# Kernel tuning notes

Hardware: AMD Instinct MI355X
Metric: run time of the kernel (lower is better)

The kernel has to match this reference:

```python
import jax, jax.numpy as jnp
import numpy as np
import itertools as it
from math import factorial

DIM, N = 3, 30
K = 2 * DIM * N + 1          # 181
P = factorial(N) // factorial(N - DIM)  # 24360
DEMB = DIM * DIM + K         # 190

# permutation index tables (trace-time constants)
_combs = np.array(list(it.permutations(range(N), DIM)), dtype=np.int32)          # (P, DIM)
_rest = np.array([sorted(set(range(N)) - set(map(int, c))) for c in _combs],
                 dtype=np.int32)                                                  # (P, N-DIM)


def setup_inputs() -> dict:
    key = jax.random.key(0)
    k0, k1, k2, k3, k4 = jax.random.split(key, 5)
    return {
        "matrix": jax.random.normal(k0, (DIM, N), dtype=jnp.float32),
        "Ws_in": jax.random.normal(k1, (K, DIM), dtype=jnp.float32),        # inner weights_sort
        "Wd_in": jax.random.normal(k2, (K, N - DIM), dtype=jnp.float32),    # inner weights_dot
        "Ws_out": jax.random.normal(k3, (K, DEMB), dtype=jnp.float32),      # outer weights_sort
        "Wd_out": jax.random.normal(k4, (K, P), dtype=jnp.float32),         # outer weights_dot
    }


def reference(matrix, Ws_in, Wd_in, Ws_out, Wd_out):
    combs = jnp.asarray(_combs)   # (P, DIM)
    rest = jnp.asarray(_rest)     # (P, N-DIM)
    cols = matrix.T               # (N, DIM) -- columns of the cloud as rows

    # UpperGram, batched over all P permutations
    Xd = cols[combs].transpose(0, 2, 1)   # (P, DIM, DIM) selected columns
    Xr = cols[rest].transpose(0, 2, 1)    # (P, DIM, N-DIM) remaining columns (sorted)
    gram = jnp.einsum('pdi,pdj->pij', Xd, Xd)          # Xd^T Xd, (P, DIM, DIM)
    # torch flattens gram.transpose(1,0); gram is exactly symmetric so this equals row-major
    gram_flat = gram.transpose(0, 2, 1).reshape(P, DIM * DIM)
    proj = jnp.einsum('pdi,pdm->pim', Xd, Xr)          # Xd^T Xrest, (P, DIM, N-DIM)

    # inner Embed (non-original branch), batched over P
    sm = jnp.einsum('pim,ki->pmk', proj, Ws_in)        # (P, N-DIM, K)
    sm_sorted = jnp.sort(sm, axis=1)                   # column-wise sort (dim=0 in torch)
    emb = jnp.einsum('km,pmk->pk', Wd_in, sm_sorted)   # diag(Wd @ sorted), (P, K)

    vec = jnp.concatenate([gram_flat, emb], axis=1)    # (P, DEMB); torch's vec before .t()

    # outer Embed (original branch) on mat = vec.T (DEMB, P)
    sm2 = vec @ Ws_out.T                               # mat^T @ Ws^T, (P, K)
    sm2_sorted = jnp.sort(sm2, axis=0)                 # sort over permutation axis
    out = jnp.einsum('kp,pk->k', Wd_out, sm2_sorted)   # diag(Wd @ sorted), (K,)
    return out
```

## Files before the change

### kernel.cpp

```cpp
#include <hip/hip_runtime.h>
#include <hip/hip_bf16.h>

#define DIMK 3
#define NPTS 30
#define KK   181
#define PP   24360
#define DEMB 190
#define VLD  192
#define SNP  24576
#define SNPS 24608

typedef __attribute__((ext_vector_type(8))) short bf16x8;
typedef __attribute__((ext_vector_type(4))) float f32x4;
typedef __attribute__((ext_vector_type(2))) __fp16 h2;
typedef __attribute__((ext_vector_type(4))) ushort u16x4;
typedef __attribute__((ext_vector_type(4))) unsigned u32x4;

__device__ __forceinline__ ushort f2bf(float f) {
    unsigned u = __float_as_uint(f);
    u += 0x7FFFu + ((u >> 16) & 1u);
    return (ushort)(u >> 16);
}

__global__ __launch_bounds__(1024, 2) void k_inner(
    const float* __restrict__ M,
    const float* __restrict__ Ws_in,
    const float* __restrict__ Wd_in,
    const float* __restrict__ Wout,
    ushort* __restrict__ Abf,
    ushort* __restrict__ vec)
{
    __shared__ float Gs[NPTS * 32];
    __shared__ float WsS[192 * 3];
    __shared__ float WdS[192 * 28];

    const int tid = threadIdx.x;

    {
        int gid = blockIdx.x * 1024 + tid;
        if (gid < 192 * 192) {
            int k = gid / 192, d = gid - k * 192;
            Abf[gid] = (k < KK && d < DEMB) ? f2bf(Wout[k * DEMB + d]) : (ushort)0;
        }
    }

    for (int i = tid; i < 192 * 3; i += 1024) WsS[i] = (i < KK * 3) ? Ws_in[i] : 0.f;
    for (int i = tid; i < 192 * 28; i += 1024) {
        int k = i / 28, m = i - k * 28;
        WdS[i] = (k < KK && m < 27) ? Wd_in[k * 27 + m] : 0.f;
    }
    for (int e = tid; e < NPTS * 32; e += 1024) {
        int a = e >> 5, b = e & 31;
        Gs[e] = (b < NPTS)
            ? (M[a] * M[b] + M[NPTS + a] * M[NPTS + b] + M[2 * NPTS + a] * M[2 * NPTS + b])
            : 0.f;
    }
    __syncthreads();

    const int wave = __builtin_amdgcn_readfirstlane(tid >> 6);
    const int lane = tid & 63;
    const int wid = blockIdx.x * 16 + wave;
    const int chunk = wid % 3;
    const int pstream = wid / 3;
    const int nstream = (chunk == 2) ? 2730 : 2731;
    const int k = chunk * 64 + lane;

    const float INF = __builtin_inff();
    const bool kvalid = (k < KK);
    const float w0 = WsS[k * 3 + 0];
    const float w1 = WsS[k * 3 + 1];
    const float w2 = WsS[k * 3 + 2];
    const float* wd = WdS + k * 28;

    const int NPAIR = PP / 2;

    for (int t = pstream; t < NPAIR; t += nstream) {
        const int p0 = 2 * t;
        int i0 = p0 / 812;
        int r  = p0 - i0 * 812;
        int i1 = r / 28;
        int i2 = r - i1 * 28;
        int c0 = i0;
        int c1 = i1 + (i1 >= c0 ? 1 : 0);
        int lo = min(c0, c1), hi = max(c0, c1);
        int c2a = i2;
        if (c2a >= lo) c2a++;
        if (c2a >= hi) c2a++;
        int c2b = i2 + 1;
        if (c2b >= lo) c2b++;
        if (c2b >= hi) c2b++;

        ushort* vrow0 = vec + (long)p0 * VLD;
        ushort* vrow1 = vrow0 + VLD;

        if (chunk == 0 && lane < 9) {
            int i = lane / 3, j = lane % 3;
            int cia = (i == 0) ? c0 : ((i == 1) ? c1 : c2a);
            int cja = (j == 0) ? c0 : ((j == 1) ? c1 : c2a);
            vrow0[lane] = f2bf(Gs[(cia << 5) + cja]);
            int cib = (i == 0) ? c0 : ((i == 1) ? c1 : c2b);
            int cjb = (j == 0) ? c0 : ((j == 1) ? c1 : c2b);
            vrow1[lane] = f2bf(Gs[(cib << 5) + cjb]);
        }

        const float* g0 = Gs + (c0 << 5);
        const float* g1 = Gs + (c1 << 5);
        const float* ga = Gs + (c2a << 5);
        const float* gb = Gs + (c2b << 5);
        const unsigned basem = (1u << c0) | (1u << c1);
        const unsigned maska = basem | (1u << c2a);
        const unsigned maskb = basem | (1u << c2b);

        h2 s[30];
#pragma unroll
        for (int q = 0; q < 8; ++q) {
            float4 x0 = *(const float4*)&g0[q * 4];
            float4 x1 = *(const float4*)&g1[q * 4];
            float4 xa = *(const float4*)&ga[q * 4];
            float4 xb = *(const float4*)&gb[q * 4];
            int j0 = q * 4;
            if (j0 + 0 < NPTS) {
                float c = w0 * x0.x + w1 * x1.x;
                float va = w2 * xa.x + c;
                float vb = w2 * xb.x + c;
                va = ((maska >> (j0 + 0)) & 1u) ? INF : va;
                vb = ((maskb >> (j0 + 0)) & 1u) ? INF : vb;
                s[j0 + 0] = __builtin_amdgcn_cvt_pkrtz(va, vb);
            }
            if (j0 + 1 < NPTS) {
                float c = w0 * x0.y + w1 * x1.y;
                float va = w2 * xa.y + c;
                float vb = w2 * xb.y + c;
                va = ((maska >> (j0 + 1)) & 1u) ? INF : va;
                vb = ((maskb >> (j0 + 1)) & 1u) ? INF : vb;
                s[j0 + 1] = __builtin_amdgcn_cvt_pkrtz(va, vb);
            }
            if (j0 + 2 < NPTS) {
                float c = w0 * x0.z + w1 * x1.z;
                float va = w2 * xa.z + c;
                float vb = w2 * xb.z + c;
                va = ((maska >> (j0 + 2)) & 1u) ? INF : va;
                vb = ((maskb >> (j0 + 2)) & 1u) ? INF : vb;
                s[j0 + 2] = __builtin_amdgcn_cvt_pkrtz(va, vb);
            }
            if (j0 + 3 < NPTS) {
                float c = w0 * x0.w + w1 * x1.w;
                float va = w2 * xa.w + c;
                float vb = w2 * xb.w + c;
                va = ((maska >> (j0 + 3)) & 1u) ? INF : va;
                vb = ((maskb >> (j0 + 3)) & 1u) ? INF : vb;
                s[j0 + 3] = __builtin_amdgcn_cvt_pkrtz(va, vb);
            }
        }

#pragma unroll
        for (int pw = 1; pw < 32; pw <<= 1) {
#pragma unroll
            for (int kk = pw; kk >= 1; kk >>= 1) {
#pragma unroll
                for (int j = kk % pw; j + kk < 32; j += 2 * kk) {
#pragma unroll
                    for (int i = 0; i < kk; ++i) {
                        int a = i + j, b = i + j + kk;
                        if (a / (pw * 2) == b / (pw * 2) && b < 30
                            && !(pw == 16 && a == 27)) {
                            h2 x = s[a], y = s[b];
                            s[a] = __builtin_elementwise_min(x, y);
                            s[b] = __builtin_elementwise_max(x, y);
                        }
                    }
                }
            }
        }

        if (kvalid) {
            float emb0 = 0.f, emb1 = 0.f;
#pragma unroll
            for (int j = 0; j < 24; j += 4) {
                float4 w4 = *(const float4*)&wd[j];
                emb0 += w4.x * (float)s[j + 0].x + w4.y * (float)s[j + 1].x
                      + w4.z * (float)s[j + 2].x + w4.w * (float)s[j + 3].x;
                emb1 += w4.x * (float)s[j + 0].y + w4.y * (float)s[j + 1].y
                      + w4.z * (float)s[j + 2].y + w4.w * (float)s[j + 3].y;
            }
            {
                float4 w4 = *(const float4*)&wd[24];
                emb0 += w4.x * (float)s[24].x + w4.y * (float)s[25].x
                      + w4.z * (float)s[26].x;
                emb1 += w4.x * (float)s[24].y + w4.y * (float)s[25].y
                      + w4.z * (float)s[26].y;
            }
            vrow0[9 + k] = f2bf(emb0);
            vrow1[9 + k] = f2bf(emb1);
        } else if (k < 183) {
            vrow0[9 + k] = 0;
            vrow1[9 + k] = 0;
        }
    }
}

__global__ __launch_bounds__(256) void k_gemm(
    const ushort* __restrict__ vecB,
    const ushort* __restrict__ Abf,
    ushort* __restrict__ sm2TP)
{
    const int tid  = threadIdx.x;
    const int bid  = blockIdx.x;
    const int tile = bid >> 2;
    const int qtr  = bid & 3;
    const int wave = tid >> 6;
    const int lane = tid & 63;
    const int n = lane & 15;
    const int quad = lane >> 4;

    const int prow = tile * 64 + wave * 16 + n;
    bf16x8 afrag[6];
    {
        const ushort* row = vecB + (size_t)prow * VLD;
#pragma unroll
        for (int kc = 0; kc < 6; ++kc)
            afrag[kc] = *(const bf16x8*)&row[kc * 32 + quad * 8];
    }

    const int pb = tile * 64 + wave * 16 + quad * 4;

#pragma unroll
    for (int i = 0; i < 3; ++i) {
        const int kt = qtr * 3 + i;
        const int kg = kt * 16 + n;
        f32x4 acc = {0.f, 0.f, 0.f, 0.f};
        const ushort* arow = Abf + kg * 192;
#pragma unroll
        for (int kc = 0; kc < 6; ++kc) {
            bf16x8 bfrag = *(const bf16x8*)&arow[kc * 32 + quad * 8];
            acc = __builtin_amdgcn_mfma_f32_16x16x32_bf16(afrag[kc], bfrag, acc, 0, 0, 0);
        }
        if (kg < KK) {
            u16x4 st;
#pragma unroll
            for (int r = 0; r < 4; ++r) {
                int p = pb + r;
                unsigned e;
                if (p < PP) {
                    unsigned u = __float_as_uint(acc[r]);
                    u = (u & 0x80000000u) ? ~u : (u | 0x80000000u);
                    e = (u + 0x8000u) >> 16;
                } else {
                    e = 0xFFFFu;
                }
                st[r] = (ushort)e;
            }
            *(u16x4*)&sm2TP[(size_t)kg * SNPS + pb] = st;
        }
    }
}

__global__ __launch_bounds__(1024, 1) void k_hist(
    const ushort* __restrict__ sm2TP,
    const float* __restrict__ WdOut,
    float* __restrict__ out)
{
    __shared__ unsigned hist[16384];
    __shared__ ushort sv[SNP];
    __shared__ unsigned wred[16];
    __shared__ float fred[16];

    const int tid  = threadIdx.x;
    const int wave = tid >> 6;
    const int lane = tid & 63;
    const int k    = blockIdx.x;

    const ushort* rowU = sm2TP + (size_t)k * SNPS;
    const float* wrow  = WdOut + (size_t)k * PP;

    u16x4 kv[6];
#pragma unroll
    for (int j = 0; j < 6; ++j)
        kv[j] = *(const u16x4*)&rowU[tid * 4 + j * 4096];

    unsigned below = 0;
    for (int p2 = 0; p2 < 2; ++p2) {
        const unsigned kbase = (unsigned)p2 << 15;

        for (int i = tid; i < 4096; i += 1024)
            ((u32x4*)hist)[i] = (u32x4){0u, 0u, 0u, 0u};
        __syncthreads();

#pragma unroll
        for (int j = 0; j < 6; ++j) {
#pragma unroll
            for (int e = 0; e < 4; ++e) {
                unsigned u = kv[j][e];
                unsigned rel = u - kbase;
                if (rel < 32768u) {
                    unsigned wd = rel >> 1;
                    atomicAdd(&hist[((wd & 15u) << 10) + (wd >> 4)],
                              1u << ((rel & 1u) << 4));
                }
            }
        }
        __syncthreads();

        unsigned w[16];
        unsigned tsum = 0;
#pragma unroll
        for (int i = 0; i < 16; ++i) {
            w[i] = hist[(i << 10) + tid];
            tsum += (w[i] & 0xFFFFu) + (w[i] >> 16);
        }
        unsigned inc = tsum;
#pragma unroll
        for (int off = 1; off < 64; off <<= 1) {
            unsigned o = (unsigned)__shfl_up((int)inc, off, 64);
            if (lane >= off) inc += o;
        }
        if (lane == 63) wred[wave] = inc;
        __syncthreads();
        unsigned wbase = 0, tot = 0;
#pragma unroll
        for (int ww = 0; ww < 16; ++ww) {
            unsigned t = wred[ww];
            tot += t;
            wbase += (ww < wave) ? t : 0u;
        }

        unsigned running = below + wbase + (inc - tsum);
#pragma unroll
        for (int i = 0; i < 16; ++i) {
            unsigned lob = running;
            running += (w[i] & 0xFFFFu);
            unsigned hib = running;
            running += (w[i] >> 16);
            hist[(i << 10) + tid] = lob | (hib << 16);
        }
        __syncthreads();

#pragma unroll
        for (int j = 0; j < 6; ++j) {
#pragma unroll
            for (int e = 0; e < 4; ++e) {
                unsigned u = kv[j][e];
                unsigned rel = u - kbase;
                if (rel < 32768u) {
                    unsigned wd = rel >> 1;
                    unsigned sh = (rel & 1u) << 4;
                    unsigned old = atomicAdd(&hist[((wd & 15u) << 10) + (wd >> 4)],
                                             1u << sh);
                    unsigned r = (old >> sh) & 0xFFFFu;
                    unsigned raw16 = (u & 0x8000u) ? (u & 0x7FFFu)
                                                   : ((~u) & 0xFFFFu);
                    sv[r] = (ushort)raw16;
                }
            }
        }
        below += tot;
        __syncthreads();
    }

    float acc = 0.f;
#pragma unroll
    for (int j = 0; j < 6; ++j) {
        int i4 = tid * 4 + j * 4096;
        if (i4 < PP) {
            u16x4 s4 = *(const u16x4*)&sv[i4];
            float4 w4 = *(const float4*)&wrow[i4];
            acc += w4.x * __uint_as_float((unsigned)s4[0] << 16)
                 + w4.y * __uint_as_float((unsigned)s4[1] << 16)
                 + w4.z * __uint_as_float((unsigned)s4[2] << 16)
                 + w4.w * __uint_as_float((unsigned)s4[3] << 16);
        }
    }

#pragma unroll
    for (int off = 32; off > 0; off >>= 1)
        acc += __shfl_down(acc, off, 64);
    if (lane == 0) fred[wave] = acc;
    __syncthreads();
    if (tid == 0) {
        float t = 0.f;
#pragma unroll
        for (int ww = 0; ww < 16; ++ww) t += fred[ww];
        out[k] = t;
    }
}

extern "C" void kernel_launch(void* const* d_in, const int* in_sizes, int n_in,
                              void* d_out, int out_size, void* d_ws, size_t ws_size,
                              hipStream_t stream) {
    const float* M      = (const float*)d_in[0];
    const float* Ws_in  = (const float*)d_in[1];
    const float* Wd_in  = (const float*)d_in[2];
    const float* Ws_out = (const float*)d_in[3];
    const float* Wd_out = (const float*)d_in[4];
    float* out = (float*)d_out;

    char* ws = (char*)d_ws;
    ushort* vecB  = (ushort*)ws;
    ushort* Abf   = (ushort*)(ws + (size_t)PP * VLD * 2);
    ushort* sm2TP = (ushort*)(ws + (size_t)PP * VLD * 2 + (size_t)192 * 192 * 2);

    k_inner<<<512, 1024, 0, stream>>>(M, Ws_in, Wd_in, Ws_out, Abf, vecB);

    k_gemm<<<(SNP / 64) * 4, 256, 0, stream>>>(vecB, Abf, sm2TP);

    k_hist<<<KK, 1024, 0, stream>>>(sm2TP, Wd_out, out);
}
```

Measured before the change: 160.4 us.

## Split per-row counting sort across four blocks by key range with atomic output

The histogram/counting-sort kernel now runs four blocks per output row. Each block handles one quarter of the 16-bit key range, so it needs a smaller histogram and a single pass. Each block counts the keys below its range to find its offset, scatters only its own keys, and dots them against the matching slice of Wd_out. Partial results are combined with atomicAdd into an output zeroed by the GEMM kernel. This raises parallelism from 181 blocks to 724 and cuts shared memory per block, at the cost of every block re-reading the full row and a non-deterministic float accumulation order.

```diff
diff --git a/kernel.cpp b/kernel.cpp
--- a/kernel.cpp
+++ b/kernel.cpp
@@ -202,7 +202,8 @@
 __global__ __launch_bounds__(256) void k_gemm(
     const ushort* __restrict__ vecB,
     const ushort* __restrict__ Abf,
-    ushort* __restrict__ sm2TP)
+    ushort* __restrict__ sm2TP,
+    float* __restrict__ out)
 {
     const int tid  = threadIdx.x;
     const int bid  = blockIdx.x;
@@ -212,6 +213,8 @@
     const int lane = tid & 63;
     const int n = lane & 15;
     const int quad = lane >> 4;
+
+    if (bid == 0 && tid < KK) out[tid] = 0.f;
 
     const int prow = tile * 64 + wave * 16 + n;
     bf16x8 afrag[6];
@@ -255,132 +258,128 @@
     }
 }
 
-__global__ __launch_bounds__(1024, 1) void k_hist(
+__global__ __launch_bounds__(1024, 8) void k_hist(
     const ushort* __restrict__ sm2TP,
     const float* __restrict__ WdOut,
     float* __restrict__ out)
 {
-    __shared__ unsigned hist[16384];
+    __shared__ unsigned hist[8192];
     __shared__ ushort sv[SNP];
-    __shared__ unsigned wred[16];
-    __shared__ float fred[16];
+    unsigned* scr = (unsigned*)sv;
 
     const int tid  = threadIdx.x;
     const int wave = tid >> 6;
     const int lane = tid & 63;
-    const int k    = blockIdx.x;
+    const int k = blockIdx.x >> 2;
+    const int q = blockIdx.x & 3;
+    const unsigned qbase = (unsigned)q << 14;
 
     const ushort* rowU = sm2TP + (size_t)k * SNPS;
     const float* wrow  = WdOut + (size_t)k * PP;
 
+    for (int i = tid; i < 2048; i += 1024)
+        ((u32x4*)hist)[i] = (u32x4){0u, 0u, 0u, 0u};
+    __syncthreads();
+
     u16x4 kv[6];
-#pragma unroll
-    for (int j = 0; j < 6; ++j)
+    unsigned below = 0;
+#pragma unroll
+    for (int j = 0; j < 6; ++j) {
         kv[j] = *(const u16x4*)&rowU[tid * 4 + j * 4096];
-
-    unsigned below = 0;
-    for (int p2 = 0; p2 < 2; ++p2) {
-        const unsigned kbase = (unsigned)p2 << 15;
-
-        for (int i = tid; i < 4096; i += 1024)
-            ((u32x4*)hist)[i] = (u32x4){0u, 0u, 0u, 0u};
-        __syncthreads();
-
-#pragma unroll
-        for (int j = 0; j < 6; ++j) {
-#pragma unroll
-            for (int e = 0; e < 4; ++e) {
-                unsigned u = kv[j][e];
-                unsigned rel = u - kbase;
-                if (rel < 32768u) {
-                    unsigned wd = rel >> 1;
-                    atomicAdd(&hist[((wd & 15u) << 10) + (wd >> 4)],
-                              1u << ((rel & 1u) << 4));
-                }
-            }
-        }
-        __syncthreads();
-
-        unsigned w[16];
-        unsigned tsum = 0;
-#pragma unroll
-        for (int i = 0; i < 16; ++i) {
-            w[i] = hist[(i << 10) + tid];
-            tsum += (w[i] & 0xFFFFu) + (w[i] >> 16);
-        }
-        unsigned inc = tsum;
-#pragma unroll
-        for (int off = 1; off < 64; off <<= 1) {
-            unsigned o = (unsigned)__shfl_up((int)inc, off, 64);
-            if (lane >= off) inc += o;
-        }
-        if (lane == 63) wred[wave] = inc;
-        __syncthreads();
-        unsigned wbase = 0, tot = 0;
-#pragma unroll
-        for (int ww = 0; ww < 16; ++ww) {
-            unsigned t = wred[ww];
-            tot += t;
-            wbase += (ww < wave) ? t : 0u;
-        }
-
-        unsigned running = below + wbase + (inc - tsum);
-#pragma unroll
-        for (int i = 0; i < 16; ++i) {
-            unsigned lob = running;
-            running += (w[i] & 0xFFFFu);
-            unsigned hib = running;
-            running += (w[i] >> 16);
-            hist[(i << 10) + tid] = lob | (hib << 16);
-        }
-        __syncthreads();
-
-#pragma unroll
-        for (int j = 0; j < 6; ++j) {
-#pragma unroll
-            for (int e = 0; e < 4; ++e) {
-                unsigned u = kv[j][e];
-                unsigned rel = u - kbase;
-                if (rel < 32768u) {
-                    unsigned wd = rel >> 1;
-                    unsigned sh = (rel & 1u) << 4;
-                    unsigned old = atomicAdd(&hist[((wd & 15u) << 10) + (wd >> 4)],
-                                             1u << sh);
-                    unsigned r = (old >> sh) & 0xFFFFu;
-                    unsigned raw16 = (u & 0x8000u) ? (u & 0x7FFFu)
-                                                   : ((~u) & 0xFFFFu);
-                    sv[r] = (ushort)raw16;
-                }
-            }
-        }
-        below += tot;
-        __syncthreads();
-    }
+#pragma unroll
+        for (int e = 0; e < 4; ++e) {
+            unsigned u = kv[j][e];
+            unsigned rel = u - qbase;
+            if (rel < 16384u) {
+                unsigned wd = rel >> 1;
+                atomicAdd(&hist[((wd & 7u) << 10) + (wd >> 3)],
+                          1u << ((rel & 1u) << 4));
+            } else {
+                below += (u < qbase) ? 1u : 0u;
+            }
+        }
+    }
+#pragma unroll
+    for (int off = 32; off > 0; off >>= 1)
+        below += (unsigned)__shfl_down((int)below, off, 64);
+    if (lane == 0) scr[wave] = below;
+    __syncthreads();
+    unsigned below_tot = 0;
+#pragma unroll
+    for (int ww = 0; ww < 16; ++ww) below_tot += scr[ww];
+    __syncthreads();
+
+    unsigned w[8];
+    unsigned tsum = 0;
+#pragma unroll
+    for (int i = 0; i < 8; ++i) {
+        w[i] = hist[(i << 10) + tid];
+        tsum += (w[i] & 0xFFFFu) + (w[i] >> 16);
+    }
+    unsigned inc = tsum;
+#pragma unroll
+    for (int off = 1; off < 64; off <<= 1) {
+        unsigned o = (unsigned)__shfl_up((int)inc, off, 64);
+        if (lane >= off) inc += o;
+    }
+    if (lane == 63) scr[wave] = inc;
+    __syncthreads();
+    unsigned wbase = 0, tot = 0;
+#pragma unroll
+    for (int ww = 0; ww < 16; ++ww) {
+        unsigned t = scr[ww];
+        tot += t;
+        wbase += (ww < wave) ? t : 0u;
+    }
+    __syncthreads();
+
+    unsigned running = wbase + (inc - tsum);
+#pragma unroll
+    for (int i = 0; i < 8; ++i) {
+        unsigned lob = running;
+        running += (w[i] & 0xFFFFu);
+        unsigned hib = running;
+        running += (w[i] >> 16);
+        hist[(i << 10) + tid] = lob | (hib << 16);
+    }
+    __syncthreads();
+
+#pragma unroll
+    for (int j = 0; j < 6; ++j) {
+#pragma unroll
+        for (int e = 0; e < 4; ++e) {
+            unsigned u = kv[j][e];
+            unsigned rel = u - qbase;
+            if (rel < 16384u) {
+                unsigned wd = rel >> 1;
+                unsigned sh = (rel & 1u) << 4;
+                unsigned old = atomicAdd(&hist[((wd & 7u) << 10) + (wd >> 3)],
+                                         1u << sh);
+                unsigned r = (old >> sh) & 0xFFFFu;
+                unsigned raw16 = (u & 0x8000u) ? (u & 0x7FFFu)
+                                               : ((~u) & 0xFFFFu);
+                sv[r] = (ushort)raw16;
+            }
+        }
+    }
+    __syncthreads();
 
     float acc = 0.f;
-#pragma unroll
-    for (int j = 0; j < 6; ++j) {
-        int i4 = tid * 4 + j * 4096;
-        if (i4 < PP) {
-            u16x4 s4 = *(const u16x4*)&sv[i4];
-            float4 w4 = *(const float4*)&wrow[i4];
-            acc += w4.x * __uint_as_float((unsigned)s4[0] << 16)
-                 + w4.y * __uint_as_float((unsigned)s4[1] << 16)
-                 + w4.z * __uint_as_float((unsigned)s4[2] << 16)
-                 + w4.w * __uint_as_float((unsigned)s4[3] << 16);
-        }
-    }
+    int cap = min((int)tot, PP - (int)below_tot);
+    for (int i = tid; i < cap; i += 1024)
+        acc += wrow[below_tot + i] * __uint_as_float((unsigned)sv[i] << 16);
 
 #pragma unroll
     for (int off = 32; off > 0; off >>= 1)
         acc += __shfl_down(acc, off, 64);
-    if (lane == 0) fred[wave] = acc;
+    __syncthreads();
+    if (lane == 0) ((float*)scr)[wave] = acc;
     __syncthreads();
     if (tid == 0) {
         float t = 0.f;
 #pragma unroll
-        for (int ww = 0; ww < 16; ++ww) t += fred[ww];
-        out[k] = t;
+        for (int ww = 0; ww < 16; ++ww) t += ((float*)scr)[ww];
+        atomicAdd(&out[k], t);
     }
 }
 
@@ -401,7 +400,7 @@
 
     k_inner<<<512, 1024, 0, stream>>>(M, Ws_in, Wd_in, Ws_out, Abf, vecB);
 
-    k_gemm<<<(SNP / 64) * 4, 256, 0, stream>>>(vecB, Abf, sm2TP);
-
-    k_hist<<<KK, 1024, 0, stream>>>(sm2TP, Wd_out, out);
+    k_gemm<<<(SNP / 64) * 4, 256, 0, stream>>>(vecB, Abf, sm2TP, out);
+
+    k_hist<<<KK * 4, 1024, 0, stream>>>(sm2TP, Wd_out, out);
 }
```

Result: slower. 229.0 us (+42.8%).
